# Kernel tuning notes

Measured on AMD Instinct MI355X. Metric: run time of the kernel, lower is better.

## Reference

```python
import jax, jax.numpy as jnp
import numpy as np

B, L, D, H = 4, 4096, 1024, 16
Dh = D // H
DECAY_INIT, DECAY_RANGE = 5.0, 1.0
LN_EPS = 1e-5


def setup_inputs() -> dict:
    key = jax.random.key(0)
    ks = jax.random.split(key, 5)
    s = 1.0 / np.sqrt(D)
    x = jax.random.normal(ks[0], (B, L, D), dtype=jnp.float32)
    Wq = jax.random.normal(ks[1], (D, D), dtype=jnp.float32) * s
    Wv = jax.random.normal(ks[2], (D, D), dtype=jnp.float32) * s
    Wo = jax.random.normal(ks[3], (D, D), dtype=jnp.float32) * s
    Wg = jax.random.normal(ks[4], (D, D), dtype=jnp.float32) * s
    # per-head decay logits, matching __init__: 5.0 + 1.0 * h / H
    beta = DECAY_INIT + DECAY_RANGE * (jnp.arange(H, dtype=jnp.float32) / H)
    ln_gamma = jnp.ones((D,), dtype=jnp.float32)
    ln_beta = jnp.zeros((D,), dtype=jnp.float32)
    return {"x": x, "Wq": Wq, "Wv": Wv, "Wo": Wo, "Wg": Wg,
            "beta": beta, "ln_gamma": ln_gamma, "ln_beta": ln_beta}


def _retention_scan(v, lam):
    # v: (B,L,H,Dh), lam: (H,); s_t = lam * s_{t-1} + v_t  (s_{-1} = 0)
    a = jnp.broadcast_to(lam[None, None, :, None], v.shape)

    def combine(c1, c2):
        a1, b1 = c1
        a2, b2 = c2
        return a1 * a2, a2 * b1 + b2

    _, s = jax.lax.associative_scan(combine, (a, v), axis=1)
    return s


def _layernorm(x, gamma, beta):
    mu = jnp.mean(x, axis=-1, keepdims=True)
    var = jnp.mean(jnp.square(x - mu), axis=-1, keepdims=True)
    return (x - mu) * jax.lax.rsqrt(var + LN_EPS) * gamma + beta


def reference(x, Wq, Wv, Wo, Wg, beta, ln_gamma, ln_beta):
    b, l, d = x.shape
    # decay lambda per head: (1 - 2^-beta) clamped to (tiny, 1 - 1e-9)
    tiny = jnp.finfo(jnp.float32).tiny
    lam = jnp.clip(1.0 - jnp.exp2(-beta), tiny, 1.0 - 1e-9)
    q = (x @ Wq.T).reshape(b, l, H, Dh)
    v = (x @ Wv.T).reshape(b, l, H, Dh)
    state = _retention_scan(v, lam)             # (B,L,H,Dh)
    ret = (q * state).reshape(b, l, d)          # per-timestep retention readout
    y = _layernorm(ret, ln_gamma, ln_beta)
    g = jax.nn.silu(x @ Wg.T)                   # swish gate
    out = (y * g) @ Wo.T
    return out
```

## Files before the change

kernel.cpp:

```cpp
#include <hip/hip_runtime.h>
#include <hip/hip_bf16.h>
#include <cfloat>

#define BB 4
#define LL 4096
#define DD 1024
#define HH 16
#define DHH 64
#define MM (BB * LL)
#define LN_EPS 1e-5f
#define LDQVG 3072
#define SCC 16
#define NCHUNK (LL / SCC)

typedef __hip_bfloat16 bf16;
typedef __attribute__((ext_vector_type(8))) short short8;
typedef __attribute__((ext_vector_type(16))) float float16_t;

struct bf16x4 { bf16 a, b, c, d; };
struct alignas(16) bf8 { bf16 e[8]; };

__device__ __forceinline__ float b2f(bf16 u) {
    union { unsigned int i; float f; } c;
    c.i = ((unsigned int)__bfloat16_as_ushort(u)) << 16;
    return c.f;
}

__device__ __forceinline__ float lam_of(const float* beta, int head) {
    float lam = 1.0f - exp2f(-beta[head]);
    return fminf(fmaxf(lam, 1.1754944e-38f), 1.0f - 1e-9f);
}

__global__ __launch_bounds__(256) void cvt_all(const float* __restrict__ x,
                                               const float* __restrict__ wq,
                                               const float* __restrict__ wv,
                                               const float* __restrict__ wg,
                                               const float* __restrict__ wo,
                                               bf16* __restrict__ xb,
                                               bf16* __restrict__ wb) {
    const int blk = blockIdx.x;
    const float* src;
    bf16* dst;
    size_t off;
    if (blk < 16384) {
        src = x; dst = xb; off = (size_t)blk * 1024;
    } else {
        int wblk  = blk - 16384;
        int which = wblk >> 10;
        src = (which == 0) ? wq : (which == 1) ? wv : (which == 2) ? wg : wo;
        dst = wb + (size_t)which * 1048576;
        off = (size_t)(wblk & 1023) * 1024;
    }
    size_t i = off + threadIdx.x * 4;
    float4 f = *(const float4*)(src + i);
    bf16x4 o;
    o.a = __float2bfloat16(f.x);
    o.b = __float2bfloat16(f.y);
    o.c = __float2bfloat16(f.z);
    o.d = __float2bfloat16(f.w);
    *(bf16x4*)(dst + i) = o;
}

__device__ __forceinline__ void async16(const bf16* g, bf16* l) {
    __builtin_amdgcn_global_load_lds(
        (const __attribute__((address_space(1))) void*)g,
        (__attribute__((address_space(3))) void*)l,
        16, 0, 0);
}

template <typename OutT, int KK>
__global__ __launch_bounds__(256) void gemm_bt(const bf16* __restrict__ A,
                                               const bf16* __restrict__ Bm,
                                               OutT* __restrict__ C,
                                               int M, int N, int ldc) {
    __shared__ bf16 sA[128 * 64];
    __shared__ bf16 sB[128 * 64];

    const int t    = threadIdx.x;
    const int lane = t & 63;
    const int wave = t >> 6;
    const int wm   = (wave >> 1) * 64;
    const int wn   = (wave & 1) * 64;

    const int bm = blockIdx.x;
    const int bn = blockIdx.y;

    const bf16* gA[4];
    const bf16* gB[4];
    bf16* lA[4];
    bf16* lB[4];
#pragma unroll
    for (int j = 0; j < 4; ++j) {
        int c = t + j * 256;
        int r = c >> 3;
        int g = ((c & 7) - (r & 7)) & 7;
        gA[j] = A  + (size_t)(bm * 128 + r) * KK + g * 8;
        gB[j] = Bm + (size_t)(bn * 128 + r) * KK + g * 8;
        lA[j] = sA + c * 8;
        lB[j] = sB + c * 8;
    }

    const int kh = lane >> 5;
    const bf16* rdA[2][4];
    const bf16* rdB[2][4];
#pragma unroll
    for (int mi = 0; mi < 2; ++mi) {
        int r = wm + (lane & 31) + mi * 32;
#pragma unroll
        for (int tk = 0; tk < 4; ++tk) {
            int kc = tk * 2 + kh;
            rdA[mi][tk] = sA + (r * 8 + ((kc + r) & 7)) * 8;
        }
    }
#pragma unroll
    for (int ni = 0; ni < 2; ++ni) {
        int r = wn + (lane & 31) + ni * 32;
#pragma unroll
        for (int tk = 0; tk < 4; ++tk) {
            int kc = tk * 2 + kh;
            rdB[ni][tk] = sB + (r * 8 + ((kc + r) & 7)) * 8;
        }
    }

    float16_t acc[2][2] = {};

#pragma unroll 1
    for (int it = 0; it < KK / 64; ++it) {
#pragma unroll
        for (int j = 0; j < 4; ++j) async16(gA[j], lA[j]);
#pragma unroll
        for (int j = 0; j < 4; ++j) async16(gB[j], lB[j]);
#pragma unroll
        for (int j = 0; j < 4; ++j) { gA[j] += 64; gB[j] += 64; }
        __syncthreads();

#pragma unroll
        for (int tk = 0; tk < 4; ++tk) {
            short8 a0 = *(const short8*)rdA[0][tk];
            short8 a1 = *(const short8*)rdA[1][tk];
            short8 b0 = *(const short8*)rdB[0][tk];
            short8 b1 = *(const short8*)rdB[1][tk];
            acc[0][0] = __builtin_amdgcn_mfma_f32_32x32x16_bf16(a0, b0, acc[0][0], 0, 0, 0);
            acc[0][1] = __builtin_amdgcn_mfma_f32_32x32x16_bf16(a0, b1, acc[0][1], 0, 0, 0);
            acc[1][0] = __builtin_amdgcn_mfma_f32_32x32x16_bf16(a1, b0, acc[1][0], 0, 0, 0);
            acc[1][1] = __builtin_amdgcn_mfma_f32_32x32x16_bf16(a1, b1, acc[1][1], 0, 0, 0);
        }
        __syncthreads();
    }

    const int col0 = bn * 128 + wn + (lane & 31);
    const int row0 = bm * 128 + wm + 4 * (lane >> 5);
#pragma unroll
    for (int mi = 0; mi < 2; ++mi) {
#pragma unroll
        for (int ni = 0; ni < 2; ++ni) {
#pragma unroll
            for (int reg = 0; reg < 16; ++reg) {
                int row = row0 + mi * 32 + (reg & 3) + 8 * (reg >> 2);
                C[(size_t)row * ldc + col0 + ni * 32] = (OutT)acc[mi][ni][reg];
            }
        }
    }
}

__global__ __launch_bounds__(64) void scan_chunksum(const bf16* __restrict__ qvg,
                                                    const float* __restrict__ beta,
                                                    float* __restrict__ S) {
    const int c    = blockIdx.x;
    const int half = blockIdx.y;
    const int b    = blockIdx.z;
    const int tid  = threadIdx.x;
    const int dh0  = half * 512 + tid * 8;
    const float lam = lam_of(beta, dh0 >> 6);

    const bf16* vp = qvg + 1024 + ((size_t)(b * LL + c * SCC)) * LDQVG + dh0;

    float s[8] = {};
#pragma unroll
    for (int t = 0; t < SCC; ++t) {
        bf8 vv = *(const bf8*)(vp + (size_t)t * LDQVG);
#pragma unroll
        for (int j = 0; j < 8; ++j)
            s[j] = fmaf(s[j], lam, b2f(vv.e[j]));
    }

    float* sp = S + ((size_t)(b * NCHUNK + c)) * DD + dh0;
    float4 lo = {s[0], s[1], s[2], s[3]};
    float4 hi = {s[4], s[5], s[6], s[7]};
    *(float4*)(sp)     = lo;
    *(float4*)(sp + 4) = hi;
}

__global__ __launch_bounds__(64) void scan_carry(const float* __restrict__ S,
                                                 float* __restrict__ T,
                                                 const float* __restrict__ beta) {
    const int gid = blockIdx.x * 64 + threadIdx.x;
    const int b = gid >> 10;
    const int f = gid & 1023;
    const float lam  = lam_of(beta, f >> 6);
    const float lamC = powf(lam, (float)SCC);

    const size_t base = (size_t)b * NCHUNK * DD + f;

    float v[8];
#pragma unroll
    for (int j = 0; j < 8; ++j) v[j] = S[base + (size_t)j * DD];

    float t = 0.0f;
    for (int c0 = 0; c0 < NCHUNK; c0 += 8) {
        float cur[8];
#pragma unroll
        for (int j = 0; j < 8; ++j) cur[j] = v[j];
        if (c0 + 8 < NCHUNK) {
#pragma unroll
            for (int j = 0; j < 8; ++j)
                v[j] = S[base + (size_t)(c0 + 8 + j) * DD];
        }
#pragma unroll
        for (int j = 0; j < 8; ++j) {
            T[base + (size_t)(c0 + j) * DD] = t;
            t = fmaf(t, lamC, cur[j]);
        }
    }
}

__global__ __launch_bounds__(128) void scan_apply_ln(const bf16* __restrict__ qvg,
                                                     const float* __restrict__ beta,
                                                     const float* __restrict__ T,
                                                     const float* __restrict__ gamma,
                                                     const float* __restrict__ betaln,
                                                     bf16* __restrict__ z) {
    __shared__ bf16 lds_ret[SCC][DD];

    const int c   = blockIdx.x;
    const int b   = blockIdx.y;
    const int tid = threadIdx.x;
    const int f0  = tid * 8;
    const float lam = lam_of(beta, f0 >> 6);

    const float* tp = T + ((size_t)(b * NCHUNK + c)) * DD + f0;
    float4 lo = *(const float4*)(tp);
    float4 hi = *(const float4*)(tp + 4);
    float s[8] = {lo.x, lo.y, lo.z, lo.w, hi.x, hi.y, hi.z, hi.w};

    const bf16* qp = qvg + ((size_t)(b * LL + c * SCC)) * LDQVG + f0;
#pragma unroll
    for (int t = 0; t < SCC; ++t) {
        const size_t off = (size_t)t * LDQVG;
        bf8 vv = *(const bf8*)(qp + 1024 + off);
        bf8 qq = *(const bf8*)(qp + off);
        bf8 o;
#pragma unroll
        for (int j = 0; j < 8; ++j) {
            s[j] = fmaf(s[j], lam, b2f(vv.e[j]));
            o.e[j] = __float2bfloat16(b2f(qq.e[j]) * s[j]);
        }
        *(bf8*)(&lds_ret[t][f0]) = o;
    }
    __syncthreads();

    const int lane = tid & 63;
    const int wv   = tid >> 6;

    float gmA[8], btA[8], gmB[8], btB[8];
#pragma unroll
    for (int j = 0; j < 8; j += 4) {
        *(float4*)(gmA + j) = *(const float4*)(gamma  + lane * 8 + j);
        *(float4*)(btA + j) = *(const float4*)(betaln + lane * 8 + j);
        *(float4*)(gmB + j) = *(const float4*)(gamma  + 512 + lane * 8 + j);
        *(float4*)(btB + j) = *(const float4*)(betaln + 512 + lane * 8 + j);
    }

    for (int t = wv; t < SCC; t += 2) {
        bf8 rA = *(const bf8*)(&lds_ret[t][lane * 8]);
        bf8 rB = *(const bf8*)(&lds_ret[t][512 + lane * 8]);

        float xa[8], xb2[8];
        float sum = 0.f, sq = 0.f;
#pragma unroll
        for (int j = 0; j < 8; ++j) {
            xa[j]  = b2f(rA.e[j]);
            xb2[j] = b2f(rB.e[j]);
            sum += xa[j] + xb2[j];
            sq  += xa[j] * xa[j] + xb2[j] * xb2[j];
        }
#pragma unroll
        for (int off = 32; off >= 1; off >>= 1) {
            sum += __shfl_xor(sum, off, 64);
            sq  += __shfl_xor(sq,  off, 64);
        }
        const float mu   = sum * (1.0f / DD);
        const float var  = sq * (1.0f / DD) - mu * mu;
        const float rstd = rsqrtf(var + LN_EPS);

        const size_t row = (size_t)(b * LL + c * SCC + t);
        const bf16* gp = qvg + row * LDQVG + 2048 + lane * 8;
        bf8 gA = *(const bf8*)(gp);
        bf8 gB = *(const bf8*)(gp + 512);

        bf8 oA, oB;
#pragma unroll
        for (int j = 0; j < 8; ++j) {
            float ya = (xa[j]  - mu) * rstd * gmA[j] + btA[j];
            float yb = (xb2[j] - mu) * rstd * gmB[j] + btB[j];
            float ga = b2f(gA.e[j]);
            float gb = b2f(gB.e[j]);
            oA.e[j] = __float2bfloat16(ya * (ga / (1.0f + expf(-ga))));
            oB.e[j] = __float2bfloat16(yb * (gb / (1.0f + expf(-gb))));
        }
        bf16* zp = z + row * DD + lane * 8;
        *(bf8*)(zp)       = oA;
        *(bf8*)(zp + 512) = oB;
    }
}

extern "C" void kernel_launch(void* const* d_in, const int* in_sizes, int n_in,
                              void* d_out, int out_size, void* d_ws, size_t ws_size,
                              hipStream_t stream) {
    const float* x     = (const float*)d_in[0];
    const float* Wq    = (const float*)d_in[1];
    const float* Wv    = (const float*)d_in[2];
    const float* Wo    = (const float*)d_in[3];
    const float* Wg    = (const float*)d_in[4];
    const float* beta  = (const float*)d_in[5];
    const float* ln_g  = (const float*)d_in[6];
    const float* ln_b  = (const float*)d_in[7];
    float* out = (float*)d_out;

    char* ws = (char*)d_ws;
    bf16*  xb   = (bf16*)ws;
    float* Sbuf = (float*)ws;
    bf16*  wqb  = (bf16*)(ws + (size_t)32 * 1024 * 1024);
    float* Tbuf = (float*)(ws + (size_t)32 * 1024 * 1024);
    bf16*  wob  = wqb + 3 * 1048576;
    bf16*  qvg  = (bf16*)(ws + (size_t)40 * 1024 * 1024);
    bf16*  zb   = xb;

    cvt_all<<<dim3(16384 + 4096), dim3(256), 0, stream>>>(x, Wq, Wv, Wg, Wo, xb, wqb);

    gemm_bt<bf16, DD><<<dim3(MM / 128, LDQVG / 128), dim3(256), 0, stream>>>(
        xb, wqb, qvg, MM, LDQVG, LDQVG);

    scan_chunksum<<<dim3(NCHUNK, 2, BB), dim3(64), 0, stream>>>(qvg, beta, Sbuf);
    scan_carry<<<dim3(64), dim3(64), 0, stream>>>(Sbuf, Tbuf, beta);
    scan_apply_ln<<<dim3(NCHUNK, BB), dim3(128), 0, stream>>>(
        qvg, beta, Tbuf, ln_g, ln_b, zb);

    gemm_bt<float, DD><<<dim3(MM / 128, DD / 128), dim3(256), 0, stream>>>(
        zb, wob, out, MM, DD, DD);
}
```

Measured before the change: 350.5 us.

## Replace GEMM with 256x256-tile, 4-stage async-LDS pipelined MFMA kernel

Replaces the 128x128 single-buffered GEMM with a 256x256-tile kernel using 512 threads, BK=32, and a four-slot LDS ring. Global-to-LDS async copies are issued three tiles ahead and paced with explicit vmcnt waits and barriers. The MFMAs move from 32x32x16 to 16x16x32 and are wrapped in setprio. The goal is to hide memory latency behind compute and raise arithmetic intensity per block. In exchange it adds many registers for the 8x4 accumulator tiles, fewer blocks (a tail effect on the small 1024-column GEMM), and fragile hand-counted synchronisation.

New measurement: 362.5 us. +3.4%, slower.

```diff
diff --git a/kernel.cpp b/kernel.cpp
--- a/kernel.cpp
+++ b/kernel.cpp
@@ -15,7 +15,7 @@
 
 typedef __hip_bfloat16 bf16;
 typedef __attribute__((ext_vector_type(8))) short short8;
-typedef __attribute__((ext_vector_type(16))) float float16_t;
+typedef __attribute__((ext_vector_type(4))) float f32x4;
 
 struct bf16x4 { bf16 a, b, c, d; };
 struct alignas(16) bf8 { bf16 e[8]; };
@@ -69,95 +69,108 @@
 }
 
 template <typename OutT, int KK>
-__global__ __launch_bounds__(256) void gemm_bt(const bf16* __restrict__ A,
-                                               const bf16* __restrict__ Bm,
-                                               OutT* __restrict__ C,
-                                               int M, int N, int ldc) {
-    __shared__ bf16 sA[128 * 64];
-    __shared__ bf16 sB[128 * 64];
+__global__ __launch_bounds__(512, 2) void gemm256(const bf16* __restrict__ A,
+                                                  const bf16* __restrict__ Bm,
+                                                  OutT* __restrict__ C,
+                                                  int ldc) {
+    constexpr int BK   = 32;
+    constexpr int NT   = KK / BK;
+    constexpr int SLOT = 256 * BK;
+
+    __shared__ alignas(16) bf16 sA[4 * SLOT];
+    __shared__ alignas(16) bf16 sB[4 * SLOT];
 
     const int t    = threadIdx.x;
     const int lane = t & 63;
     const int wave = t >> 6;
-    const int wm   = (wave >> 1) * 64;
-    const int wn   = (wave & 1) * 64;
-
-    const int bm = blockIdx.x;
-    const int bn = blockIdx.y;
-
-    const bf16* gA[4];
-    const bf16* gB[4];
-    bf16* lA[4];
-    bf16* lB[4];
-#pragma unroll
-    for (int j = 0; j < 4; ++j) {
-        int c = t + j * 256;
-        int r = c >> 3;
-        int g = ((c & 7) - (r & 7)) & 7;
-        gA[j] = A  + (size_t)(bm * 128 + r) * KK + g * 8;
-        gB[j] = Bm + (size_t)(bn * 128 + r) * KK + g * 8;
-        lA[j] = sA + c * 8;
-        lB[j] = sB + c * 8;
-    }
-
-    const int kh = lane >> 5;
-    const bf16* rdA[2][4];
-    const bf16* rdB[2][4];
-#pragma unroll
-    for (int mi = 0; mi < 2; ++mi) {
-        int r = wm + (lane & 31) + mi * 32;
-#pragma unroll
-        for (int tk = 0; tk < 4; ++tk) {
-            int kc = tk * 2 + kh;
-            rdA[mi][tk] = sA + (r * 8 + ((kc + r) & 7)) * 8;
-        }
-    }
-#pragma unroll
-    for (int ni = 0; ni < 2; ++ni) {
-        int r = wn + (lane & 31) + ni * 32;
-#pragma unroll
-        for (int tk = 0; tk < 4; ++tk) {
-            int kc = tk * 2 + kh;
-            rdB[ni][tk] = sB + (r * 8 + ((kc + r) & 7)) * 8;
-        }
-    }
-
-    float16_t acc[2][2] = {};
+    const int wm   = wave >> 2;
+    const int wn   = wave & 3;
+    const int bm   = blockIdx.x;
+    const int bn   = blockIdx.y;
+
+    const int srow = t >> 2;
+    const int cswz = ((t & 3) ^ (srow & 3)) * 8;
+    const bf16* gA0 = A  + (size_t)(bm * 256 + srow) * KK + cswz;
+    const bf16* gB0 = Bm + (size_t)(bn * 256 + srow) * KK + cswz;
+    const size_t half = (size_t)128 * KK;
+    bf16* const lA = sA + t * 8;
+    bf16* const lB = sB + t * 8;
+
+    const int swz8  = ((lane >> 4) ^ (lane & 3)) * 8;
+    const int offA0 = (wm * 128 + (lane & 15)) * BK + swz8;
+    const int offB0 = (wn * 64  + (lane & 15)) * BK + swz8;
+
+    f32x4 acc[8][4] = {};
+
+#define STAGE_A(Tn) { const int sl = ((Tn) & 3) * SLOT;                  \
+    const bf16* g = gA0 + (Tn) * BK;                                     \
+    async16(g, lA + sl); async16(g + half, lA + sl + 4096); }
+#define STAGE_B(Tn) { const int sl = ((Tn) & 3) * SLOT;                  \
+    const bf16* g = gB0 + (Tn) * BK;                                     \
+    async16(g, lB + sl); async16(g + half, lB + sl + 4096); }
+
+    STAGE_A(0); STAGE_B(0);
+    STAGE_A(1); STAGE_B(1);
+    STAGE_A(2); STAGE_B(2);
+    asm volatile("s_waitcnt vmcnt(8)" ::: "memory");
+    __builtin_amdgcn_s_barrier();
+
+#define TILE(T, DOSTAGE, VMN)                                                  \
+  {                                                                            \
+    const bf16* sbA = sA + ((T) & 3) * SLOT;                                   \
+    const bf16* sbB = sB + ((T) & 3) * SLOT;                                   \
+    short8 av[4], bv[4];                                                       \
+    _Pragma("unroll") for (int i = 0; i < 4; ++i)                              \
+        av[i] = *(const short8*)(sbA + offA0 + i * 512);                       \
+    _Pragma("unroll") for (int i = 0; i < 4; ++i)                              \
+        bv[i] = *(const short8*)(sbB + offB0 + i * 512);                       \
+    if (DOSTAGE) STAGE_A((T) + 3);                                             \
+    __builtin_amdgcn_s_barrier();                                              \
+    __builtin_amdgcn_s_setprio(1);                                             \
+    _Pragma("unroll") for (int i = 0; i < 4; ++i)                              \
+      _Pragma("unroll") for (int j = 0; j < 4; ++j)                            \
+        acc[i][j] = __builtin_amdgcn_mfma_f32_16x16x32_bf16(                   \
+            av[i], bv[j], acc[i][j], 0, 0, 0);                                 \
+    __builtin_amdgcn_s_setprio(0);                                             \
+    __builtin_amdgcn_s_barrier();                                              \
+    _Pragma("unroll") for (int i = 0; i < 4; ++i)                              \
+        av[i] = *(const short8*)(sbA + offA0 + (4 + i) * 512);                 \
+    if (DOSTAGE) STAGE_B((T) + 3);                                             \
+    __builtin_amdgcn_s_barrier();                                              \
+    __builtin_amdgcn_s_setprio(1);                                             \
+    _Pragma("unroll") for (int i = 0; i < 4; ++i)                              \
+      _Pragma("unroll") for (int j = 0; j < 4; ++j)                            \
+        acc[4 + i][j] = __builtin_amdgcn_mfma_f32_16x16x32_bf16(               \
+            av[i], bv[j], acc[4 + i][j], 0, 0, 0);                             \
+    __builtin_amdgcn_s_setprio(0);                                             \
+    if ((VMN) == 8)      asm volatile("s_waitcnt vmcnt(8)" ::: "memory");      \
+    else if ((VMN) == 4) asm volatile("s_waitcnt vmcnt(4)" ::: "memory");      \
+    else if ((VMN) == 0) asm volatile("s_waitcnt vmcnt(0)" ::: "memory");      \
+    __builtin_amdgcn_s_barrier();                                              \
+  }
 
 #pragma unroll 1
-    for (int it = 0; it < KK / 64; ++it) {
-#pragma unroll
-        for (int j = 0; j < 4; ++j) async16(gA[j], lA[j]);
-#pragma unroll
-        for (int j = 0; j < 4; ++j) async16(gB[j], lB[j]);
-#pragma unroll
-        for (int j = 0; j < 4; ++j) { gA[j] += 64; gB[j] += 64; }
-        __syncthreads();
-
-#pragma unroll
-        for (int tk = 0; tk < 4; ++tk) {
-            short8 a0 = *(const short8*)rdA[0][tk];
-            short8 a1 = *(const short8*)rdA[1][tk];
-            short8 b0 = *(const short8*)rdB[0][tk];
-            short8 b1 = *(const short8*)rdB[1][tk];
-            acc[0][0] = __builtin_amdgcn_mfma_f32_32x32x16_bf16(a0, b0, acc[0][0], 0, 0, 0);
-            acc[0][1] = __builtin_amdgcn_mfma_f32_32x32x16_bf16(a0, b1, acc[0][1], 0, 0, 0);
-            acc[1][0] = __builtin_amdgcn_mfma_f32_32x32x16_bf16(a1, b0, acc[1][0], 0, 0, 0);
-            acc[1][1] = __builtin_amdgcn_mfma_f32_32x32x16_bf16(a1, b1, acc[1][1], 0, 0, 0);
-        }
-        __syncthreads();
-    }
-
-    const int col0 = bn * 128 + wn + (lane & 31);
-    const int row0 = bm * 128 + wm + 4 * (lane >> 5);
-#pragma unroll
-    for (int mi = 0; mi < 2; ++mi) {
-#pragma unroll
-        for (int ni = 0; ni < 2; ++ni) {
-#pragma unroll
-            for (int reg = 0; reg < 16; ++reg) {
-                int row = row0 + mi * 32 + (reg & 3) + 8 * (reg >> 2);
-                C[(size_t)row * ldc + col0 + ni * 32] = (OutT)acc[mi][ni][reg];
+    for (int T = 0; T < NT - 3; ++T) {
+        TILE(T, true, 8);
+    }
+    TILE(NT - 3, false, 4);
+    TILE(NT - 2, false, 0);
+    TILE(NT - 1, false, -1);
+
+#undef TILE
+#undef STAGE_A
+#undef STAGE_B
+
+    const int col0 = bn * 256 + wn * 64 + (lane & 15);
+    const int row0 = bm * 256 + wm * 128 + ((lane >> 4) * 4);
+#pragma unroll
+    for (int mi = 0; mi < 8; ++mi) {
+#pragma unroll
+        for (int ni = 0; ni < 4; ++ni) {
+#pragma unroll
+            for (int r = 0; r < 4; ++r) {
+                int row = row0 + mi * 16 + r;
+                C[(size_t)row * ldc + col0 + ni * 16] = (OutT)acc[mi][ni][r];
             }
         }
     }
@@ -338,14 +351,14 @@
 
     cvt_all<<<dim3(16384 + 4096), dim3(256), 0, stream>>>(x, Wq, Wv, Wg, Wo, xb, wqb);
 
-    gemm_bt<bf16, DD><<<dim3(MM / 128, LDQVG / 128), dim3(256), 0, stream>>>(
-        xb, wqb, qvg, MM, LDQVG, LDQVG);
+    gemm256<bf16, DD><<<dim3(MM / 256, LDQVG / 256), dim3(512), 0, stream>>>(
+        xb, wqb, qvg, LDQVG);
 
     scan_chunksum<<<dim3(NCHUNK, 2, BB), dim3(64), 0, stream>>>(qvg, beta, Sbuf);
     scan_carry<<<dim3(64), dim3(64), 0, stream>>>(Sbuf, Tbuf, beta);
     scan_apply_ln<<<dim3(NCHUNK, BB), dim3(128), 0, stream>>>(
         qvg, beta, Tbuf, ln_g, ln_b, zb);
 
-    gemm_bt<float, DD><<<dim3(MM / 128, DD / 128), dim3(256), 0, stream>>>(
-        zb, wob, out, MM, DD, DD);
-}
+    gemm256<float, DD><<<dim3(MM / 256, DD / 256), dim3(512), 0, stream>>>(
+        zb, wob, out, DD);
+}
```

## Replace GEMM with 256x128 triple-buffered async-LDS ring pipeline

Applied to the files above, without the earlier changes.

Replaces the single-buffered 128x128 BK=64 GEMM with a 256x128 tile, BK=32 kernel that uses a three-slot LDS ring. Global-to-LDS async loads for later tiles are issued while the current tile's MFMAs run, with one barrier per iteration and s_setprio around the MFMA block. A new XOR swizzle replaces the old LDS layout to keep reads conflict-free. The larger tile raises per-wave accumulator pressure (8 accumulators of 16 floats each), which may hurt occupancy despite the launch bound of 2.

Result: no change. 348.4 us (-0.6%).

```diff
diff --git a/kernel.cpp b/kernel.cpp
--- a/kernel.cpp
+++ b/kernel.cpp
@@ -69,89 +69,116 @@
 }
 
 template <typename OutT, int KK>
-__global__ __launch_bounds__(256) void gemm_bt(const bf16* __restrict__ A,
-                                               const bf16* __restrict__ Bm,
-                                               OutT* __restrict__ C,
-                                               int M, int N, int ldc) {
-    __shared__ bf16 sA[128 * 64];
-    __shared__ bf16 sB[128 * 64];
+__global__ __launch_bounds__(256, 2) void gemm_ring(const bf16* __restrict__ A,
+                                                    const bf16* __restrict__ Bm,
+                                                    OutT* __restrict__ C,
+                                                    int ldc) {
+    constexpr int BK    = 32;
+    constexpr int NT    = KK / BK;
+    constexpr int ASLOT = 256 * BK;
+    constexpr int BSLOT = 128 * BK;
+
+    __shared__ alignas(16) bf16 sA[3 * ASLOT];
+    __shared__ alignas(16) bf16 sB[3 * BSLOT];
 
     const int t    = threadIdx.x;
     const int lane = t & 63;
     const int wave = t >> 6;
-    const int wm   = (wave >> 1) * 64;
-    const int wn   = (wave & 1) * 64;
-
-    const int bm = blockIdx.x;
-    const int bn = blockIdx.y;
-
-    const bf16* gA[4];
-    const bf16* gB[4];
-    bf16* lA[4];
-    bf16* lB[4];
-#pragma unroll
-    for (int j = 0; j < 4; ++j) {
-        int c = t + j * 256;
-        int r = c >> 3;
-        int g = ((c & 7) - (r & 7)) & 7;
-        gA[j] = A  + (size_t)(bm * 128 + r) * KK + g * 8;
-        gB[j] = Bm + (size_t)(bn * 128 + r) * KK + g * 8;
-        lA[j] = sA + c * 8;
-        lB[j] = sB + c * 8;
-    }
+    const int wm   = wave >> 1;
+    const int wn   = wave & 1;
+    const int bm   = blockIdx.x;
+    const int bn   = blockIdx.y;
+
+    const int srow = t >> 2;
+    const int cswz = ((t & 3) ^ ((srow >> 1) & 3)) * 8;
+    const bf16* gA = A  + (size_t)(bm * 256 + srow) * KK + cswz;
+    const bf16* gB = Bm + (size_t)(bn * 128 + srow) * KK + cswz;
+    const size_t rstep = (size_t)64 * KK;
+    bf16* const lA = sA + t * 8;
+    bf16* const lB = sB + t * 8;
 
     const int kh = lane >> 5;
-    const bf16* rdA[2][4];
-    const bf16* rdB[2][4];
-#pragma unroll
-    for (int mi = 0; mi < 2; ++mi) {
-        int r = wm + (lane & 31) + mi * 32;
-#pragma unroll
-        for (int tk = 0; tk < 4; ++tk) {
-            int kc = tk * 2 + kh;
-            rdA[mi][tk] = sA + (r * 8 + ((kc + r) & 7)) * 8;
-        }
-    }
-#pragma unroll
-    for (int ni = 0; ni < 2; ++ni) {
-        int r = wn + (lane & 31) + ni * 32;
-#pragma unroll
-        for (int tk = 0; tk < 4; ++tk) {
-            int kc = tk * 2 + kh;
-            rdB[ni][tk] = sB + (r * 8 + ((kc + r) & 7)) * 8;
-        }
-    }
-
-    float16_t acc[2][2] = {};
+    const int f  = ((lane & 31) >> 1) & 3;
+    const bf16* rdA[4][2];
+    const bf16* rdB[2][2];
+#pragma unroll
+    for (int mi = 0; mi < 4; ++mi)
+#pragma unroll
+        for (int kk = 0; kk < 2; ++kk) {
+            const int row = wm * 128 + mi * 32 + (lane & 31);
+            rdA[mi][kk] = sA + row * BK + (((2 * kk + kh) ^ f) * 8);
+        }
+#pragma unroll
+    for (int ni = 0; ni < 2; ++ni)
+#pragma unroll
+        for (int kk = 0; kk < 2; ++kk) {
+            const int row = wn * 64 + ni * 32 + (lane & 31);
+            rdB[ni][kk] = sB + row * BK + (((2 * kk + kh) ^ f) * 8);
+        }
+
+    float16_t acc[4][2] = {};
+
+    int slR = 0,         slR2 = 0;
+    int slS = 2 * ASLOT, slS2 = 2 * BSLOT;
+
+#pragma unroll
+    for (int j = 0; j < 4; ++j) async16(gA + j * rstep, lA + j * 2048);
+#pragma unroll
+    for (int j = 0; j < 2; ++j) async16(gB + j * rstep, lB + j * 2048);
+    gA += BK; gB += BK;
+#pragma unroll
+    for (int j = 0; j < 4; ++j) async16(gA + j * rstep, lA + ASLOT + j * 2048);
+#pragma unroll
+    for (int j = 0; j < 2; ++j) async16(gB + j * rstep, lB + BSLOT + j * 2048);
+    gA += BK; gB += BK;
+    asm volatile("s_waitcnt vmcnt(6)" ::: "memory");
+    __builtin_amdgcn_s_barrier();
+
+#define TILE(DOSTAGE, VMN)                                                     \
+  {                                                                            \
+    short8 a[4][2], b[2][2];                                                   \
+    _Pragma("unroll") for (int mi = 0; mi < 4; ++mi)                           \
+      _Pragma("unroll") for (int kk = 0; kk < 2; ++kk)                         \
+        a[mi][kk] = *(const short8*)(rdA[mi][kk] + slR);                       \
+    _Pragma("unroll") for (int ni = 0; ni < 2; ++ni)                           \
+      _Pragma("unroll") for (int kk = 0; kk < 2; ++kk)                         \
+        b[ni][kk] = *(const short8*)(rdB[ni][kk] + slR2);                      \
+    if (DOSTAGE) {                                                             \
+      _Pragma("unroll") for (int j = 0; j < 4; ++j)                            \
+          async16(gA + j * rstep, lA + slS + j * 2048);                        \
+      _Pragma("unroll") for (int j = 0; j < 2; ++j)                            \
+          async16(gB + j * rstep, lB + slS2 + j * 2048);                       \
+      gA += BK; gB += BK;                                                      \
+    }                                                                          \
+    __builtin_amdgcn_s_setprio(1);                                             \
+    _Pragma("unroll") for (int kk = 0; kk < 2; ++kk)                           \
+      _Pragma("unroll") for (int mi = 0; mi < 4; ++mi)                         \
+        _Pragma("unroll") for (int ni = 0; ni < 2; ++ni)                       \
+          acc[mi][ni] = __builtin_amdgcn_mfma_f32_32x32x16_bf16(               \
+              a[mi][kk], b[ni][kk], acc[mi][ni], 0, 0, 0);                     \
+    __builtin_amdgcn_s_setprio(0);                                             \
+    if ((VMN) == 6)      asm volatile("s_waitcnt vmcnt(6)" ::: "memory");      \
+    else if ((VMN) == 0) asm volatile("s_waitcnt vmcnt(0)" ::: "memory");      \
+    if ((VMN) >= 0) __builtin_amdgcn_s_barrier();                              \
+    slR  = (slR  == 2 * ASLOT) ? 0 : slR  + ASLOT;                             \
+    slR2 = (slR2 == 2 * BSLOT) ? 0 : slR2 + BSLOT;                             \
+    slS  = (slS  == 2 * ASLOT) ? 0 : slS  + ASLOT;                             \
+    slS2 = (slS2 == 2 * BSLOT) ? 0 : slS2 + BSLOT;                             \
+  }
 
 #pragma unroll 1
-    for (int it = 0; it < KK / 64; ++it) {
-#pragma unroll
-        for (int j = 0; j < 4; ++j) async16(gA[j], lA[j]);
-#pragma unroll
-        for (int j = 0; j < 4; ++j) async16(gB[j], lB[j]);
-#pragma unroll
-        for (int j = 0; j < 4; ++j) { gA[j] += 64; gB[j] += 64; }
-        __syncthreads();
-
-#pragma unroll
-        for (int tk = 0; tk < 4; ++tk) {
-            short8 a0 = *(const short8*)rdA[0][tk];
-            short8 a1 = *(const short8*)rdA[1][tk];
-            short8 b0 = *(const short8*)rdB[0][tk];
-            short8 b1 = *(const short8*)rdB[1][tk];
-            acc[0][0] = __builtin_amdgcn_mfma_f32_32x32x16_bf16(a0, b0, acc[0][0], 0, 0, 0);
-            acc[0][1] = __builtin_amdgcn_mfma_f32_32x32x16_bf16(a0, b1, acc[0][1], 0, 0, 0);
-            acc[1][0] = __builtin_amdgcn_mfma_f32_32x32x16_bf16(a1, b0, acc[1][0], 0, 0, 0);
-            acc[1][1] = __builtin_amdgcn_mfma_f32_32x32x16_bf16(a1, b1, acc[1][1], 0, 0, 0);
-        }
-        __syncthreads();
-    }
-
-    const int col0 = bn * 128 + wn + (lane & 31);
-    const int row0 = bm * 128 + wm + 4 * (lane >> 5);
-#pragma unroll
-    for (int mi = 0; mi < 2; ++mi) {
+    for (int T = 0; T < NT - 2; ++T) {
+        TILE(true, 6);
+    }
+    TILE(false, 0);
+    TILE(false, -1);
+
+#undef TILE
+
+    const int col0 = bn * 128 + wn * 64 + (lane & 31);
+    const int row0 = bm * 256 + wm * 128 + 4 * (lane >> 5);
+#pragma unroll
+    for (int mi = 0; mi < 4; ++mi) {
 #pragma unroll
         for (int ni = 0; ni < 2; ++ni) {
 #pragma unroll
@@ -338,14 +365,14 @@
 
     cvt_all<<<dim3(16384 + 4096), dim3(256), 0, stream>>>(x, Wq, Wv, Wg, Wo, xb, wqb);
 
-    gemm_bt<bf16, DD><<<dim3(MM / 128, LDQVG / 128), dim3(256), 0, stream>>>(
-        xb, wqb, qvg, MM, LDQVG, LDQVG);
+    gemm_ring<bf16, DD><<<dim3(MM / 256, LDQVG / 128), dim3(256), 0, stream>>>(
+        xb, wqb, qvg, LDQVG);
 
     scan_chunksum<<<dim3(NCHUNK, 2, BB), dim3(64), 0, stream>>>(qvg, beta, Sbuf);
     scan_carry<<<dim3(64), dim3(64), 0, stream>>>(Sbuf, Tbuf, beta);
     scan_apply_ln<<<dim3(NCHUNK, BB), dim3(128), 0, stream>>>(
         qvg, beta, Tbuf, ln_g, ln_b, zb);
 
-    gemm_bt<float, DD><<<dim3(MM / 128, DD / 128), dim3(256), 0, stream>>>(
-        zb, wob, out, MM, DD, DD);
-}
+    gemm_ring<float, DD><<<dim3(MM / 256, DD / 128), dim3(256), 0, stream>>>(
+        zb, wob, out, DD);
+}
```
